# Optimization experiments

Measured on AMD Instinct MI355X. Metric: run time of the kernel, lower is better.

## Reference

```python
import jax, jax.numpy as jnp
import numpy as np


def _build_transform():
    # Deterministic re-creation of SegmentationAugmentation.build_3d_transform
    # with flip=True, offset=0.1, scale=0.2, rotate=True.
    rng = np.random.default_rng(0)
    t = np.eye(4, dtype=np.float32)
    for i in range(3):
        if rng.random() > 0.5:
            t[i, i] *= -1.0
        t[i, 3] = 0.1 * (rng.random() * 2.0 - 1.0)
        t[i, i] *= 1.0 + 0.2 * (rng.random() * 2.0 - 1.0)
    a = rng.random() * 2.0 * np.pi
    s, c = np.sin(a), np.cos(a)
    rot = np.array([[c, -s, 0, 0], [s, c, 0, 0], [0, 0, 1, 0], [0, 0, 0, 1]],
                   dtype=np.float32)
    return t @ rot


def _affine_grid(theta, size):
    # theta: [B,3,4]; size: (B,C,D,H,W); align_corners=False.
    B, C, D, H, W = size
    def lin(n):
        # pixel-center normalized coords: (2i+1)/n - 1
        return (2.0 * jnp.arange(n, dtype=jnp.float32) + 1.0) / n - 1.0
    z, y, x = jnp.meshgrid(lin(D), lin(H), lin(W), indexing='ij')
    pts = jnp.stack([x, y, z], axis=-1)  # [D,H,W,3], (x,y,z) order as in torch
    return (jnp.einsum('bij,dhwj->bdhwi', theta[:, :, :3], pts)
            + theta[:, None, None, None, :, 3])


def _grid_sample_3d_border(inp, grid):
    # trilinear grid_sample, padding_mode='border', align_corners=False.
    # inp: [B,C,D,H,W]; grid: [B,Do,Ho,Wo,3] with (x,y,z) normalized coords.
    B, C, D, H, W = inp.shape
    Do, Ho, Wo = grid.shape[1:4]

    def unnorm(cn, n):
        # align_corners=False unnormalize, then border clamp
        return jnp.clip(((cn + 1.0) * n - 1.0) * 0.5, 0.0, n - 1.0)

    x = unnorm(grid[..., 0], W)
    y = unnorm(grid[..., 1], H)
    z = unnorm(grid[..., 2], D)
    x0 = jnp.floor(x); y0 = jnp.floor(y); z0 = jnp.floor(z)
    fx, fy, fz = x - x0, y - y0, z - z0
    x0i = x0.astype(jnp.int32); y0i = y0.astype(jnp.int32); z0i = z0.astype(jnp.int32)
    x1i = jnp.minimum(x0i + 1, W - 1)
    y1i = jnp.minimum(y0i + 1, H - 1)
    z1i = jnp.minimum(z0i + 1, D - 1)

    inp_flat = inp.reshape(B, C, D * H * W)
    N = Do * Ho * Wo
    out = jnp.zeros((B, C, N), dtype=inp.dtype)
    for zi, wz in ((z0i, 1.0 - fz), (z1i, fz)):
        for yi, wy in ((y0i, 1.0 - fy), (y1i, fy)):
            for xi, wx in ((x0i, 1.0 - fx), (x1i, fx)):
                idx = ((zi * H + yi) * W + xi).reshape(B, 1, N)
                v = jnp.take_along_axis(
                    inp_flat, jnp.broadcast_to(idx, (B, C, N)), axis=2)
                w = (wz * wy * wx).reshape(B, 1, N)
                out = out + v * w
    return out.reshape(B, C, Do, Ho, Wo)


def setup_inputs() -> dict:
    key = jax.random.key(0)
    k1, k2 = jax.random.split(key)
    input_g = jax.random.normal(k1, (8, 1, 128, 128, 128), dtype=jnp.float32)
    label_g = jax.random.uniform(k2, (8, 1, 128, 128, 128), dtype=jnp.float32)
    transform = jnp.asarray(_build_transform())
    return {"input_g": input_g, "label_g": label_g, "transform": transform}


def reference(input_g, label_g, transform):
    # transpose(-3,-1): swap depth and width axes
    inp = jnp.swapaxes(input_g, -3, -1)
    lab = jnp.swapaxes(label_g, -3, -1)
    B = inp.shape[0]
    theta = jnp.broadcast_to(transform[:3][None], (B, 3, 4)).astype(jnp.float32)
    grid = _affine_grid(theta, inp.shape)
    aug_inp = _grid_sample_3d_border(inp, grid)
    aug_lab = _grid_sample_3d_border(lab, grid)
    aug_inp = jnp.swapaxes(aug_inp, -3, -1)
    aug_lab = jnp.swapaxes(aug_lab, -3, -1)
    return aug_inp, aug_lab > 0.5
```

## Files before the change

kernel.cpp:

```cpp
#include <hip/hip_runtime.h>


#define NV 128
#define TOTAL (8 * NV * NV * NV)

__global__ __launch_bounds__(128) void seg_aug_tables(
    const float* __restrict__ T, float* __restrict__ ws)
{
#pragma clang fp contract(off)
    const int t = threadIdx.x;
    if (blockIdx.x == 128) {
        float p4 = (2.0f * (float)t + 1.0f) / 128.0f - 1.0f;
        float uz = T[10] * p4 + T[11];
        float gz = ((uz + 1.0f) * 128.0f - 1.0f) * 0.5f;
        gz = fminf(fmaxf(gz, 0.0f), 127.0f);
        float fz0f = floorf(gz);
        float fz = gz - fz0f;
        int2 v;
        v.x = (int)fz0f;
        v.y = __float_as_int(fz);
        ((int2*)ws)[t] = v;
    } else {
        const int idx = blockIdx.x * 128 + t;
        const int o3 = idx & (NV - 1);
        const int o2 = idx >> 7;
        float p2 = (2.0f * (float)o2 + 1.0f) / 128.0f - 1.0f;
        float p3 = (2.0f * (float)o3 + 1.0f) / 128.0f - 1.0f;
        float ux = (T[0] * p2 + T[1] * p3) + T[3];
        float uy = (T[4] * p2 + T[5] * p3) + T[7];
        float gx = ((ux + 1.0f) * 128.0f - 1.0f) * 0.5f;
        float gy = ((uy + 1.0f) * 128.0f - 1.0f) * 0.5f;
        gx = fminf(fmaxf(gx, 0.0f), 127.0f);
        gy = fminf(fmaxf(gy, 0.0f), 127.0f);
        float fx0f = floorf(gx), fy0f = floorf(gy);
        int4 v;
        v.x = (int)fx0f;
        v.y = (int)fy0f;
        v.z = __float_as_int(gx - fx0f);
        v.w = __float_as_int(gy - fy0f);
        ((int4*)(ws + 256))[idx] = v;
    }
}

__global__ __launch_bounds__(128) void seg_aug_kernel(
    const float* __restrict__ in,
    const float* __restrict__ lab,
    const float* __restrict__ ws,
    float* __restrict__ out_in,
    float* __restrict__ out_lab)
{
#pragma clang fp contract(off)
    __shared__ __align__(16) float s[8 * NV + 1];

    const int t = threadIdx.x;
    const int b = blockIdx.x >> 14;

    const int4 e = ((const int4*)(ws + 256))[blockIdx.x & 16383];
    const int ix0 = __builtin_amdgcn_readfirstlane(e.x);
    const int iy0 = __builtin_amdgcn_readfirstlane(e.y);
    const float fx = __int_as_float(e.z);
    const float fy = __int_as_float(e.w);
    const int ix1 = min(ix0 + 1, NV - 1);
    const int iy1 = min(iy0 + 1, NV - 1);

    const int2 ze = ((const int2*)ws)[t];
    const int iz0 = ze.x;
    const float fz = __int_as_float(ze.y);

    const size_t bbase = (size_t)b << 21;
    {
        const int rid = t >> 5;
        const int seg = t & 31;
        const int ixS = (rid & 2) ? ix1 : ix0;
        const int iyS = (rid & 1) ? iy1 : iy0;
        const int off = (ixS * NV + iyS) * NV + seg * 4;
        __builtin_amdgcn_global_load_lds(in  + bbase + off, &s[t * 4],       16, 0, 0);
        __builtin_amdgcn_global_load_lds(lab + bbase + off, &s[512 + t * 4], 16, 0, 0);
    }
    if (t == 0) s[8 * NV] = 0.0f;

    const float wz0 = 1.0f - fz, wz1 = fz;
    const float wx0 = 1.0f - fx, wx1 = fx;
    const float wy0 = 1.0f - fy, wy1 = fy;

    __syncthreads();

    const float* rp = s + iz0;
    float ia00 = rp[0 * NV], ib00 = rp[0 * NV + 1];
    float ia01 = rp[1 * NV], ib01 = rp[1 * NV + 1];
    float ia10 = rp[2 * NV], ib10 = rp[2 * NV + 1];
    float ia11 = rp[3 * NV], ib11 = rp[3 * NV + 1];
    float la00 = rp[4 * NV], lb00 = rp[4 * NV + 1];
    float la01 = rp[5 * NV], lb01 = rp[5 * NV + 1];
    float la10 = rp[6 * NV], lb10 = rp[6 * NV + 1];
    float la11 = rp[7 * NV], lb11 = rp[7 * NV + 1];

    float tz0y0 = wz0 * wy0, tz0y1 = wz0 * wy1;
    float tz1y0 = wz1 * wy0, tz1y1 = wz1 * wy1;
    float w1 = tz0y0 * wx0, w2 = tz0y0 * wx1;
    float w3 = tz0y1 * wx0, w4 = tz0y1 * wx1;
    float w5 = tz1y0 * wx0, w6 = tz1y0 * wx1;
    float w7 = tz1y1 * wx0, w8 = tz1y1 * wx1;

    float acc_i = 0.0f;
    acc_i = acc_i + ia00 * w1;
    acc_i = acc_i + ia10 * w2;
    acc_i = acc_i + ia01 * w3;
    acc_i = acc_i + ia11 * w4;
    acc_i = acc_i + ib00 * w5;
    acc_i = acc_i + ib10 * w6;
    acc_i = acc_i + ib01 * w7;
    acc_i = acc_i + ib11 * w8;

    float acc_l = 0.0f;
    acc_l = acc_l + la00 * w1;
    acc_l = acc_l + la10 * w2;
    acc_l = acc_l + la01 * w3;
    acc_l = acc_l + la11 * w4;
    acc_l = acc_l + lb00 * w5;
    acc_l = acc_l + lb10 * w6;
    acc_l = acc_l + lb01 * w7;
    acc_l = acc_l + lb11 * w8;

    const int oidx = blockIdx.x * NV + t;
    out_in[oidx]  = acc_i;
    out_lab[oidx] = (acc_l > 0.5f) ? 1.0f : 0.0f;
}

extern "C" void kernel_launch(void* const* d_in, const int* in_sizes, int n_in,
                              void* d_out, int out_size, void* d_ws, size_t ws_size,
                              hipStream_t stream) {
    const float* in  = (const float*)d_in[0];
    const float* lab = (const float*)d_in[1];
    const float* T   = (const float*)d_in[2];
    float* out_in  = (float*)d_out;
    float* out_lab = (float*)d_out + TOTAL;
    float* ws      = (float*)d_ws;

    seg_aug_tables<<<dim3(129), dim3(128), 0, stream>>>(T, ws);
    seg_aug_kernel<<<dim3(TOTAL / 128), dim3(128), 0, stream>>>(
        in, lab, ws, out_in, out_lab);
}
```

Measured before the change: 248.0 us.

## Assign one output column per wavefront, replacing block barrier with per-wave waitcnt

Each 64-lane wavefront now owns one output column and gets its own LDS region. It loads its four source rows for input and label, then waits with s_waitcnt vmcnt(0) instead of __syncthreads. Each lane produces two z outputs, and blocks grow to 512 threads covering eight columns. The aim is to drop block-wide barriers and reduce per-block launch and scheduling overhead, at the cost of more LDS per block and less per-thread parallelism.

```diff
diff --git a/kernel.cpp b/kernel.cpp
--- a/kernel.cpp
+++ b/kernel.cpp
@@ -3,6 +3,8 @@
 
 #define NV 128
 #define TOTAL (8 * NV * NV * NV)
+#define WPB 8
+#define WSTRIDE 1028
 
 __global__ __launch_bounds__(128) void seg_aug_tables(
     const float* __restrict__ T, float* __restrict__ ws)
@@ -42,7 +44,7 @@
     }
 }
 
-__global__ __launch_bounds__(128) void seg_aug_kernel(
+__global__ __launch_bounds__(512) void seg_aug_kernel(
     const float* __restrict__ in,
     const float* __restrict__ lab,
     const float* __restrict__ ws,
@@ -50,81 +52,95 @@
     float* __restrict__ out_lab)
 {
 #pragma clang fp contract(off)
-    __shared__ __align__(16) float s[8 * NV + 1];
+    __shared__ __align__(16) float s[WPB * WSTRIDE];
 
     const int t = threadIdx.x;
-    const int b = blockIdx.x >> 14;
+    const int l = t & 63;
+    const int w = __builtin_amdgcn_readfirstlane(t >> 6);
+    const int col = (blockIdx.x << 3) | w;
+    const int b = col >> 14;
 
-    const int4 e = ((const int4*)(ws + 256))[blockIdx.x & 16383];
+    const int4 e = ((const int4*)(ws + 256))[col & 16383];
     const int ix0 = __builtin_amdgcn_readfirstlane(e.x);
     const int iy0 = __builtin_amdgcn_readfirstlane(e.y);
     const float fx = __int_as_float(e.z);
     const float fy = __int_as_float(e.w);
     const int ix1 = min(ix0 + 1, NV - 1);
     const int iy1 = min(iy0 + 1, NV - 1);
+    const int r00 = (ix0 * NV + iy0) * NV;
+    const int r01 = (ix0 * NV + iy1) * NV;
+    const int r10 = (ix1 * NV + iy0) * NV;
+    const int r11 = (ix1 * NV + iy1) * NV;
 
-    const int2 ze = ((const int2*)ws)[t];
-    const int iz0 = ze.x;
-    const float fz = __int_as_float(ze.y);
+    const int segoff = (l & 31) * 4;
+    const int offA = ((l < 32) ? r00 : r01) + segoff;
+    const int offB = ((l < 32) ? r10 : r11) + segoff;
+    const size_t bbase = (size_t)b << 21;
+    const float* ibp = in  + bbase;
+    const float* lbp = lab + bbase;
+    float* sw = &s[w * WSTRIDE];
+    __builtin_amdgcn_global_load_lds(ibp + offA, sw,       16, 0, 0);
+    __builtin_amdgcn_global_load_lds(ibp + offB, sw + 256, 16, 0, 0);
+    __builtin_amdgcn_global_load_lds(lbp + offA, sw + 512, 16, 0, 0);
+    __builtin_amdgcn_global_load_lds(lbp + offB, sw + 768, 16, 0, 0);
+    if (l == 0) sw[1024] = 0.0f;
 
-    const size_t bbase = (size_t)b << 21;
-    {
-        const int rid = t >> 5;
-        const int seg = t & 31;
-        const int ixS = (rid & 2) ? ix1 : ix0;
-        const int iyS = (rid & 1) ? iy1 : iy0;
-        const int off = (ixS * NV + iyS) * NV + seg * 4;
-        __builtin_amdgcn_global_load_lds(in  + bbase + off, &s[t * 4],       16, 0, 0);
-        __builtin_amdgcn_global_load_lds(lab + bbase + off, &s[512 + t * 4], 16, 0, 0);
-    }
-    if (t == 0) s[8 * NV] = 0.0f;
+    const int2 ze0 = ((const int2*)ws)[l];
+    const int2 ze1 = ((const int2*)ws)[l + 64];
 
-    const float wz0 = 1.0f - fz, wz1 = fz;
     const float wx0 = 1.0f - fx, wx1 = fx;
     const float wy0 = 1.0f - fy, wy1 = fy;
 
-    __syncthreads();
+    asm volatile("s_waitcnt vmcnt(0)" ::: "memory");
+    __builtin_amdgcn_sched_barrier(0);
 
-    const float* rp = s + iz0;
-    float ia00 = rp[0 * NV], ib00 = rp[0 * NV + 1];
-    float ia01 = rp[1 * NV], ib01 = rp[1 * NV + 1];
-    float ia10 = rp[2 * NV], ib10 = rp[2 * NV + 1];
-    float ia11 = rp[3 * NV], ib11 = rp[3 * NV + 1];
-    float la00 = rp[4 * NV], lb00 = rp[4 * NV + 1];
-    float la01 = rp[5 * NV], lb01 = rp[5 * NV + 1];
-    float la10 = rp[6 * NV], lb10 = rp[6 * NV + 1];
-    float la11 = rp[7 * NV], lb11 = rp[7 * NV + 1];
+    const int obase = col * NV;
 
-    float tz0y0 = wz0 * wy0, tz0y1 = wz0 * wy1;
-    float tz1y0 = wz1 * wy0, tz1y1 = wz1 * wy1;
-    float w1 = tz0y0 * wx0, w2 = tz0y0 * wx1;
-    float w3 = tz0y1 * wx0, w4 = tz0y1 * wx1;
-    float w5 = tz1y0 * wx0, w6 = tz1y0 * wx1;
-    float w7 = tz1y1 * wx0, w8 = tz1y1 * wx1;
+    #define DO_Z(ZE, ZOFF)                                                    \
+    {                                                                         \
+        const int iz0 = (ZE).x;                                               \
+        const float fz = __int_as_float((ZE).y);                              \
+        const float wz0 = 1.0f - fz, wz1 = fz;                                \
+        const float* rp = sw + iz0;                                           \
+        float ia00 = rp[0 * NV], ib00 = rp[0 * NV + 1];                       \
+        float ia01 = rp[1 * NV], ib01 = rp[1 * NV + 1];                       \
+        float ia10 = rp[2 * NV], ib10 = rp[2 * NV + 1];                       \
+        float ia11 = rp[3 * NV], ib11 = rp[3 * NV + 1];                       \
+        float la00 = rp[4 * NV], lb00 = rp[4 * NV + 1];                       \
+        float la01 = rp[5 * NV], lb01 = rp[5 * NV + 1];                       \
+        float la10 = rp[6 * NV], lb10 = rp[6 * NV + 1];                       \
+        float la11 = rp[7 * NV], lb11 = rp[7 * NV + 1];                       \
+        float tz0y0 = wz0 * wy0, tz0y1 = wz0 * wy1;                           \
+        float tz1y0 = wz1 * wy0, tz1y1 = wz1 * wy1;                           \
+        float w1 = tz0y0 * wx0, w2 = tz0y0 * wx1;                             \
+        float w3 = tz0y1 * wx0, w4 = tz0y1 * wx1;                             \
+        float w5 = tz1y0 * wx0, w6 = tz1y0 * wx1;                             \
+        float w7 = tz1y1 * wx0, w8 = tz1y1 * wx1;                             \
+        float acc_i = 0.0f;                                                   \
+        acc_i = acc_i + ia00 * w1;                                            \
+        acc_i = acc_i + ia10 * w2;                                            \
+        acc_i = acc_i + ia01 * w3;                                            \
+        acc_i = acc_i + ia11 * w4;                                            \
+        acc_i = acc_i + ib00 * w5;                                            \
+        acc_i = acc_i + ib10 * w6;                                            \
+        acc_i = acc_i + ib01 * w7;                                            \
+        acc_i = acc_i + ib11 * w8;                                            \
+        float acc_l = 0.0f;                                                   \
+        acc_l = acc_l + la00 * w1;                                            \
+        acc_l = acc_l + la10 * w2;                                            \
+        acc_l = acc_l + la01 * w3;                                            \
+        acc_l = acc_l + la11 * w4;                                            \
+        acc_l = acc_l + lb00 * w5;                                            \
+        acc_l = acc_l + lb10 * w6;                                            \
+        acc_l = acc_l + lb01 * w7;                                            \
+        acc_l = acc_l + lb11 * w8;                                            \
+        out_in[obase + (ZOFF)]  = acc_i;                                      \
+        out_lab[obase + (ZOFF)] = (acc_l > 0.5f) ? 1.0f : 0.0f;               \
+    }
 
-    float acc_i = 0.0f;
-    acc_i = acc_i + ia00 * w1;
-    acc_i = acc_i + ia10 * w2;
-    acc_i = acc_i + ia01 * w3;
-    acc_i = acc_i + ia11 * w4;
-    acc_i = acc_i + ib00 * w5;
-    acc_i = acc_i + ib10 * w6;
-    acc_i = acc_i + ib01 * w7;
-    acc_i = acc_i + ib11 * w8;
-
-    float acc_l = 0.0f;
-    acc_l = acc_l + la00 * w1;
-    acc_l = acc_l + la10 * w2;
-    acc_l = acc_l + la01 * w3;
-    acc_l = acc_l + la11 * w4;
-    acc_l = acc_l + lb00 * w5;
-    acc_l = acc_l + lb10 * w6;
-    acc_l = acc_l + lb01 * w7;
-    acc_l = acc_l + lb11 * w8;
-
-    const int oidx = blockIdx.x * NV + t;
-    out_in[oidx]  = acc_i;
-    out_lab[oidx] = (acc_l > 0.5f) ? 1.0f : 0.0f;
+    DO_Z(ze0, l)
+    DO_Z(ze1, l + 64)
+    #undef DO_Z
 }
 
 extern "C" void kernel_launch(void* const* d_in, const int* in_sizes, int n_in,
@@ -138,6 +154,6 @@
     float* ws      = (float*)d_ws;
 
     seg_aug_tables<<<dim3(129), dim3(128), 0, stream>>>(T, ws);
-    seg_aug_kernel<<<dim3(TOTAL / 128), dim3(128), 0, stream>>>(
+    seg_aug_kernel<<<dim3(TOTAL / NV / WPB), dim3(512), 0, stream>>>(
         in, lab, ws, out_in, out_lab);
 }
```

Measured after the change: 237.7 us. 4.1% less time.
